# Kernel tuning notes

Measured on AMD Instinct MI355X. Metric: run time of the kernel, lower is better.

Reference implementation:

```python
import jax, jax.numpy as jnp
import numpy as np

NUM_EMBEDDINGS = 1024
EMBEDDING_DIM = 256
COMMITMENT_COST = 0.25


def setup_inputs() -> dict:
    key = jax.random.key(0)
    k1, k2 = jax.random.split(key)
    inputs = jax.random.normal(k1, (32, EMBEDDING_DIM, 32, 32), dtype=jnp.float32)
    # nn.Embedding weight init: uniform(-1/K, 1/K)
    embeddings = (jax.random.uniform(k2, (NUM_EMBEDDINGS, EMBEDDING_DIM), dtype=jnp.float32) * 2.0 - 1.0) / NUM_EMBEDDINGS
    return {"inputs": inputs, "embeddings": embeddings}


def reference(inputs, embeddings):
    B, D, H, W = inputs.shape
    K = embeddings.shape[0]
    # [B,D,H,W] -> [N,D] with N = B*H*W
    flat = jnp.transpose(inputs, (0, 2, 3, 1)).reshape(-1, D)
    distances = (jnp.sum(flat * flat, axis=1, keepdims=True)
                 + jnp.sum(embeddings * embeddings, axis=1)
                 - 2.0 * jnp.matmul(flat, embeddings.T))
    encoding_indices = jnp.argmin(distances, axis=1)  # [N]
    # gather codebook vectors (same math as one-hot @ embeddings)
    quantized = embeddings[encoding_indices]  # [N,D]
    quantized = quantized.reshape(B, H, W, D).transpose(0, 3, 1, 2)  # [B,D,H,W]
    e_latent_loss = jnp.mean((jax.lax.stop_gradient(quantized) - inputs) ** 2)
    q_latent_loss = jnp.mean((quantized - jax.lax.stop_gradient(inputs)) ** 2)
    loss = q_latent_loss + COMMITMENT_COST * e_latent_loss
    # straight-through estimator
    quantized_st = inputs + jax.lax.stop_gradient(quantized - inputs)
    # perplexity from one-hot average (counts / N)
    counts = jnp.zeros((K,), dtype=flat.dtype).at[encoding_indices].add(1.0)
    avg_probs = counts / flat.shape[0]
    perplexity = jnp.exp(-jnp.sum(avg_probs * jnp.log(avg_probs + 1e-10)))
    return quantized_st, loss, perplexity, encoding_indices.reshape(B, H, W)
```

## Files before the change

### kernel.cpp

```cpp
#include <hip/hip_runtime.h>


#define NROWS 32768
#define CAPA 16384
#define CAPB 8192
#define GAP_TAU 1e-4f

typedef __attribute__((ext_vector_type(8))) short short8;
typedef __attribute__((ext_vector_type(8))) unsigned short ushort8;
typedef __attribute__((ext_vector_type(4))) float f32x4;

struct Top4 { float v0, v1, v2, v3; int i0, i1, i2; };

__device__ __forceinline__ void top4_init(Top4& t) {
    t.v0 = t.v1 = t.v2 = t.v3 = 3.4e38f;
    t.i0 = t.i1 = t.i2 = 0x7fffffff;
}
__device__ __forceinline__ void top4_insert(Top4& t, float cv, int ci) {
    if (cv < t.v3) {
        if (cv < t.v2) {
            t.v3 = t.v2;
            if (cv < t.v1) {
                t.v2 = t.v1; t.i2 = t.i1;
                if (cv < t.v0) { t.v1 = t.v0; t.i1 = t.i0; t.v0 = cv; t.i0 = ci; }
                else           { t.v1 = cv; t.i1 = ci; }
            } else { t.v2 = cv; t.i2 = ci; }
        } else { t.v3 = cv; }
    }
}
__device__ __forceinline__ void top4_merge(Top4& t, const Top4& o) {
    top4_insert(t, o.v0, o.i0);
    top4_insert(t, o.v1, o.i1);
    top4_insert(t, o.v2, o.i2);
    t.v3 = fminf(t.v3, o.v3);
}

__device__ __forceinline__ unsigned short bf16_rne(float v) {
    unsigned int u = __float_as_uint(v);
    return (unsigned short)((u + 0x7fffu + ((u >> 16) & 1u)) >> 16);
}
__device__ __forceinline__ float bf16_to_f(unsigned short h) {
    return __uint_as_float(((unsigned int)h) << 16);
}

__device__ __forceinline__ void gl16(const void* g, void* l) {
    __builtin_amdgcn_global_load_lds(
        (const __attribute__((address_space(1))) unsigned int*)g,
        (__attribute__((address_space(3))) unsigned int*)l, 16, 0, 0);
}

template <int STRIDE>
__device__ __forceinline__ float np_sumsq256(const float* __restrict__ p) {
    float half[2];
#pragma unroll
    for (int h = 0; h < 2; ++h) {
        float r[8];
#pragma unroll
        for (int j = 0; j < 8; ++j) {
            const float v = p[(size_t)(h * 128 + j) * STRIDE];
            r[j] = __fmul_rn(v, v);
        }
        for (int i = 8; i < 128; i += 8) {
#pragma unroll
            for (int j = 0; j < 8; ++j) {
                const float v = p[(size_t)(h * 128 + i + j) * STRIDE];
                r[j] = __fadd_rn(r[j], __fmul_rn(v, v));
            }
        }
        half[h] = __fadd_rn(__fadd_rn(__fadd_rn(r[0], r[1]), __fadd_rn(r[2], r[3])),
                            __fadd_rn(__fadd_rn(r[4], r[5]), __fadd_rn(r[6], r[7])));
    }
    return __fadd_rn(half[0], half[1]);
}

__global__ void prep_kernel(const float* __restrict__ emb, const float* __restrict__ x,
                            float* __restrict__ ee, float* __restrict__ xx,
                            unsigned short* __restrict__ EhT, unsigned short* __restrict__ ElT,
                            unsigned short* __restrict__ XhT, unsigned short* __restrict__ XlT,
                            float* __restrict__ wzero) {
    if (blockIdx.x >= 388) {
        for (int i = threadIdx.x; i < 1088; i += 256) wzero[i] = 0.f;
        return;
    }
    if (blockIdx.x < 4) {
        const int k = blockIdx.x * 256 + threadIdx.x;
        ee[k] = np_sumsq256<1>(emb + (size_t)k * 256);
        return;
    }
    if (blockIdx.x >= 260) {
        const int n = (blockIdx.x - 260) * 256 + threadIdx.x;
        const int b = n >> 10, p = n & 1023;
        const float* xb = x + (size_t)b * 262144 + p;
        const int kk = (n >> 1) & 3;
        float r[8];
        float half0 = 0.f, half1 = 0.f;
        for (int dc = 0; dc < 8; ++dc) {
            float v[32];
#pragma unroll
            for (int j = 0; j < 32; ++j)
                v[j] = xb[(size_t)(dc * 32 + j) * 1024];
            if ((dc & 3) == 0) {
#pragma unroll
                for (int j = 0; j < 8; ++j) r[j] = __fmul_rn(v[j], v[j]);
#pragma unroll
                for (int g = 1; g < 4; ++g)
#pragma unroll
                    for (int j = 0; j < 8; ++j)
                        r[j] = __fadd_rn(r[j], __fmul_rn(v[g * 8 + j], v[g * 8 + j]));
            } else {
#pragma unroll
                for (int g = 0; g < 4; ++g)
#pragma unroll
                    for (int j = 0; j < 8; ++j)
                        r[j] = __fadd_rn(r[j], __fmul_rn(v[g * 8 + j], v[g * 8 + j]));
            }
            if ((dc & 3) == 3) {
                const float s = __fadd_rn(
                    __fadd_rn(__fadd_rn(r[0], r[1]), __fadd_rn(r[2], r[3])),
                    __fadd_rn(__fadd_rn(r[4], r[5]), __fadd_rn(r[6], r[7])));
                if (dc == 3) half0 = s; else half1 = s;
            }
            const size_t xrow = ((size_t)dc * NROWS + n) * 32;
#pragma unroll
            for (int g = 0; g < 4; ++g) {
                ushort8 H, L;
#pragma unroll
                for (int j = 0; j < 8; ++j) {
                    const float vv = v[g * 8 + j];
                    const unsigned int u = __float_as_uint(vv);
                    H[j] = (unsigned short)(u >> 16);
                    const float rr = vv - __uint_as_float(u & 0xFFFF0000u);
                    L[j] = (unsigned short)(__float_as_uint(rr) >> 16);
                }
                *(ushort8*)(XhT + xrow + (g ^ kk) * 8) = H;
                *(ushort8*)(XlT + xrow + (g ^ kk) * 8) = L;
            }
        }
        xx[n] = __fadd_rn(half0, half1);
        return;
    }
    const int eid = (blockIdx.x - 4) * 256 + threadIdx.x;
    const int code = eid >> 6;
    const int d0 = (eid & 63) * 4;
    float4 v = *(const float4*)(emb + (size_t)code * 256 + d0);
    const float vv[4] = {v.x, v.y, v.z, v.w};
    unsigned short h[4], l[4];
#pragma unroll
    for (int i = 0; i < 4; ++i) {
        h[i] = bf16_rne(vv[i]);
        l[i] = bf16_rne(vv[i] - bf16_to_f(h[i]));
    }
    const int kk = (code >> 1) & 3;
    const int slot = (d0 & 31) >> 3;
    const int within = (d0 & 31) & 7;
    const size_t o = ((size_t)(d0 >> 5) * 1024 + code) * 32
                   + (size_t)((slot ^ kk) * 8 + within);
    *(ushort4*)(EhT + o) = make_ushort4(h[0], h[1], h[2], h[3]);
    *(ushort4*)(ElT + o) = make_ushort4(l[0], l[1], l[2], l[3]);
}

__global__ __launch_bounds__(256, 2)
void mfma_argmin_kernel(const unsigned short* __restrict__ XhT, const unsigned short* __restrict__ XlT,
                        const unsigned short* __restrict__ EhT, const unsigned short* __restrict__ ElT,
                        const float* __restrict__ ee, const float* __restrict__ xx,
                        float* __restrict__ pv0, float* __restrict__ pv1,
                        float* __restrict__ pv2, float* __restrict__ pv3,
                        int* __restrict__ pi0, int* __restrict__ pi1, int* __restrict__ pi2) {
    __shared__ __attribute__((aligned(16))) unsigned short Eh_s[2][4096];
    __shared__ __attribute__((aligned(16))) unsigned short El_s[2][4096];
    __shared__ __attribute__((aligned(16))) unsigned short Xh_s[2][4096];
    __shared__ __attribute__((aligned(16))) unsigned short Xl_s[2][4096];
    __shared__ float eeLds[128];
    __shared__ float mV0[128], mV1[128], mV2[128], mV3[128];
    __shared__ int   mI0[128], mI1[128], mI2[128];

    const int t = threadIdx.x;
    const int w = t >> 6, lane = t & 63;
    const int lane15 = lane & 15, quad = lane >> 4;
    const int nblk = blockIdx.x & 255, cblk = blockIdx.x >> 8;
    const int n0 = nblk * 128, c0 = cblk * 128;

    if (t < 128) eeLds[t] = ee[c0 + t];

    const int fslot = (quad ^ ((lane15 >> 1) & 3)) * 8;
    int eoffs[4], xoffs[4];
#pragma unroll
    for (int i = 0; i < 4; ++i)
        eoffs[i] = ((w >> 1) * 64 + i * 16 + lane15) * 32 + fslot;
#pragma unroll
    for (int j = 0; j < 4; ++j)
        xoffs[j] = ((w & 1) * 64 + j * 16 + lane15) * 32 + fslot;

    f32x4 acc[4][4];
#pragma unroll
    for (int i = 0; i < 4; ++i)
#pragma unroll
        for (int j = 0; j < 4; ++j) acc[i][j] = (f32x4){0.f, 0.f, 0.f, 0.f};

    auto STAGE = [&](int dc, int bb) {
        const size_t xoff = ((size_t)dc * NROWS + n0) * 32;
        const size_t eoff = ((size_t)dc * 1024 + c0) * 32;
#pragma unroll
        for (int k = 0; k < 2; ++k) {
            const int id = k * 256 + t;
            const int ldso = (k * 256 + w * 64) * 8;
            gl16(XhT + xoff + (size_t)id * 8, &Xh_s[bb][ldso]);
            gl16(XlT + xoff + (size_t)id * 8, &Xl_s[bb][ldso]);
            gl16(EhT + eoff + (size_t)id * 8, &Eh_s[bb][ldso]);
            gl16(ElT + eoff + (size_t)id * 8, &El_s[bb][ldso]);
        }
    };

    STAGE(0, 0);
    asm volatile("s_waitcnt vmcnt(0)" ::: "memory");
    __builtin_amdgcn_s_barrier();
    asm volatile("" ::: "memory");

#pragma unroll 2
    for (int dc = 0; dc < 8; ++dc) {
        const int bb = dc & 1;
        if (dc < 7) STAGE(dc + 1, bb ^ 1);
        short8 ah[4], al[4], bh[4], bl[4];
#pragma unroll
        for (int i = 0; i < 4; ++i) {
            ah[i] = *(const short8*)&Eh_s[bb][eoffs[i]];
            al[i] = *(const short8*)&El_s[bb][eoffs[i]];
        }
#pragma unroll
        for (int j = 0; j < 4; ++j) {
            bh[j] = *(const short8*)&Xh_s[bb][xoffs[j]];
            bl[j] = *(const short8*)&Xl_s[bb][xoffs[j]];
        }
#pragma unroll
        for (int i = 0; i < 4; ++i)
#pragma unroll
            for (int j = 0; j < 4; ++j) {
                acc[i][j] = __builtin_amdgcn_mfma_f32_16x16x32_bf16(al[i], bh[j], acc[i][j], 0, 0, 0);
                acc[i][j] = __builtin_amdgcn_mfma_f32_16x16x32_bf16(ah[i], bl[j], acc[i][j], 0, 0, 0);
                acc[i][j] = __builtin_amdgcn_mfma_f32_16x16x32_bf16(ah[i], bh[j], acc[i][j], 0, 0, 0);
            }
        asm volatile("s_waitcnt vmcnt(0)" ::: "memory");
        __builtin_amdgcn_s_barrier();
        asm volatile("" ::: "memory");
    }

    Top4 tj[4];
#pragma unroll
    for (int j = 0; j < 4; ++j) {
        const float xxv = xx[n0 + (w & 1) * 64 + j * 16 + lane15];
        Top4 tt; top4_init(tt);
#pragma unroll
        for (int i = 0; i < 4; ++i)
#pragma unroll
            for (int r = 0; r < 4; ++r) {
                const int cl = (w >> 1) * 64 + i * 16 + quad * 4 + r;
                const float t1 = __fadd_rn(xxv, eeLds[cl]);
                const float s = __fmaf_rn(-2.0f, acc[i][j][r], t1);
                top4_insert(tt, s, c0 + cl);
            }
#pragma unroll
        for (int off = 16; off <= 32; off <<= 1) {
            Top4 o;
            o.v0 = __shfl_xor(tt.v0, off, 64); o.i0 = __shfl_xor(tt.i0, off, 64);
            o.v1 = __shfl_xor(tt.v1, off, 64); o.i1 = __shfl_xor(tt.i1, off, 64);
            o.v2 = __shfl_xor(tt.v2, off, 64); o.i2 = __shfl_xor(tt.i2, off, 64);
            o.v3 = __shfl_xor(tt.v3, off, 64);
            top4_merge(tt, o);
        }
        tj[j] = tt;
    }
    if (w >= 2 && quad == 0) {
#pragma unroll
        for (int j = 0; j < 4; ++j) {
            const int idx = (w & 1) * 64 + j * 16 + lane15;
            mV0[idx] = tj[j].v0; mV1[idx] = tj[j].v1; mV2[idx] = tj[j].v2; mV3[idx] = tj[j].v3;
            mI0[idx] = tj[j].i0; mI1[idx] = tj[j].i1; mI2[idx] = tj[j].i2;
        }
    }
    __syncthreads();
    if (w < 2 && quad == 0) {
#pragma unroll
        for (int j = 0; j < 4; ++j) {
            const int idx = w * 64 + j * 16 + lane15;
            Top4 tt = tj[j];
            Top4 o;
            o.v0 = mV0[idx]; o.v1 = mV1[idx]; o.v2 = mV2[idx]; o.v3 = mV3[idx];
            o.i0 = mI0[idx]; o.i1 = mI1[idx]; o.i2 = mI2[idx];
            top4_merge(tt, o);
            mV0[idx] = tt.v0; mV1[idx] = tt.v1; mV2[idx] = tt.v2; mV3[idx] = tt.v3;
            mI0[idx] = tt.i0; mI1[idx] = tt.i1; mI2[idx] = tt.i2;
        }
    }
    __syncthreads();
    if (t < 128) {
        const size_t g = (size_t)cblk * NROWS + n0 + t;
        pv0[g] = mV0[t]; pv1[g] = mV1[t]; pv2[g] = mV2[t]; pv3[g] = mV3[t];
        pi0[g] = mI0[t]; pi1[g] = mI1[t]; pi2[g] = mI2[t];
    }
}

__global__ void combine_kernel(const float* __restrict__ pv0, const float* __restrict__ pv1,
                               const float* __restrict__ pv2, const float* __restrict__ pv3,
                               const int* __restrict__ pi0, const int* __restrict__ pi1,
                               const int* __restrict__ pi2,
                               int* __restrict__ fidx, float* __restrict__ outIdx,
                               int* __restrict__ counts,
                               int* __restrict__ listA, int* __restrict__ nA,
                               int* __restrict__ listB, int* __restrict__ nB) {
    const int n = blockIdx.x * blockDim.x + threadIdx.x;
    if (n >= NROWS) return;
    float v0[8], v1[8], v2[8]; int i0[8], i1[8], i2[8];
    float b1 = 3.4e38f, v4m = 3.4e38f;
#pragma unroll
    for (int s = 0; s < 8; ++s) {
        const size_t g = (size_t)s * NROWS + n;
        v0[s] = pv0[g]; v1[s] = pv1[g]; v2[s] = pv2[g];
        i0[s] = pi0[g]; i1[s] = pi1[g]; i2[s] = pi2[g];
        b1 = fminf(b1, v0[s]);
        v4m = fminf(v4m, pv3[g]);
    }
    if (v4m - b1 < GAP_TAU) {
        const int s = atomicAdd(nB, 1);
        if (s < CAPB) { listB[s] = n; return; }
    } else {
        int ks[24]; int cnt = 0;
#pragma unroll
        for (int s = 0; s < 8; ++s) {
            if (v0[s] - b1 < GAP_TAU) ks[cnt++] = i0[s];
            if (v1[s] - b1 < GAP_TAU) ks[cnt++] = i1[s];
            if (v2[s] - b1 < GAP_TAU) ks[cnt++] = i2[s];
        }
        if (cnt > 1) {
            const int slot = atomicAdd(nA, 1);
            if (slot < CAPA) {
                int* e = listA + (size_t)slot * 32;
                e[0] = n; e[1] = cnt;
                for (int c = 0; c < cnt; ++c) e[2 + c] = ks[c];
                return;
            }
            const int s2 = atomicAdd(nB, 1);
            if (s2 < CAPB) { listB[s2] = n; return; }
        }
        const int bi = ks[0];
        fidx[n] = bi;
        outIdx[n] = (float)bi;
        atomicAdd(&counts[bi], 1);
        return;
    }
    int bi = 0x7fffffff;
#pragma unroll
    for (int s = 0; s < 8; ++s) if (v0[s] == b1 && i0[s] < bi) bi = i0[s];
    fidx[n] = bi; outIdx[n] = (float)bi; atomicAdd(&counts[bi], 1);
}

__global__ __launch_bounds__(256)
void resolve_kernel(const float* __restrict__ x, const float* __restrict__ emb,
                    const float* __restrict__ ee, const float* __restrict__ xx,
                    const int* __restrict__ listA, const int* __restrict__ nA,
                    const int* __restrict__ listB, const int* __restrict__ nB,
                    int* __restrict__ fidx, float* __restrict__ outIdx,
                    int* __restrict__ counts) {
    __shared__ float xrow[256];
    __shared__ float bV[4];
    __shared__ int   bI[4];
    if (blockIdx.x < 512) {
        int total = *nA; if (total > CAPA) total = CAPA;
        const int sub = threadIdx.x >> 5;
        const int li  = threadIdx.x & 31;
        for (int e = blockIdx.x * 8 + sub; e < total; e += 512 * 8) {
            const int* ent = listA + (size_t)e * 32;
            const int n = ent[0], cnt = ent[1];
            float s = 3.4e38f; int k = 0x7fffffff;
            if (li < cnt) {
                k = ent[2 + li];
                const int b = n >> 10, p = n & 1023;
                const float* xr = x + (size_t)b * 262144 + p;
                const float* er = emb + (size_t)k * 256;
                float dot = 0.f;
#pragma unroll 8
                for (int d = 0; d < 256; ++d)
                    dot = __fmaf_rn(er[d], xr[(size_t)d * 1024], dot);
                s = __fmaf_rn(-2.0f, dot, __fadd_rn(xx[n], ee[k]));
            }
#pragma unroll
            for (int off = 1; off < 32; off <<= 1) {
                const float ov = __shfl_xor(s, off, 32);
                const int   ok = __shfl_xor(k, off, 32);
                if (ov < s || (ov == s && ok < k)) { s = ov; k = ok; }
            }
            if (li == 0) { fidx[n] = k; outIdx[n] = (float)k; atomicAdd(&counts[k], 1); }
        }
        return;
    }
    int total = *nB; if (total > CAPB) total = CAPB;
    for (int wq = (int)blockIdx.x - 512; wq < total; wq += 64) {
        const int n = listB[wq];
        const int b = n >> 10, p = n & 1023;
        const float* xb = x + (size_t)b * 262144 + p;
        xrow[threadIdx.x] = xb[(size_t)threadIdx.x * 1024];
        __syncthreads();
        const float xxn = xx[n];
        float best = 3.4e38f; int bi = 0x7fffffff;
        for (int k = threadIdx.x; k < 1024; k += 256) {
            const float* e = emb + (size_t)k * 256;
            float dot = 0.f;
            for (int d = 0; d < 256; ++d) dot = __fmaf_rn(e[d], xrow[d], dot);
            const float t1 = __fadd_rn(xxn, ee[k]);
            const float s = __fmaf_rn(-2.0f, dot, t1);
            if (s < best) { best = s; bi = k; }
        }
        for (int off = 32; off > 0; off >>= 1) {
            const float ov = __shfl_down(best, off, 64);
            const int   oi = __shfl_down(bi,   off, 64);
            if (ov < best || (ov == best && oi < bi)) { best = ov; bi = oi; }
        }
        const int lane = threadIdx.x & 63, wv = threadIdx.x >> 6;
        if (lane == 0) { bV[wv] = best; bI[wv] = bi; }
        __syncthreads();
        if (threadIdx.x == 0) {
            float bb = bV[0]; int ii = bI[0];
            for (int i = 1; i < 4; ++i)
                if (bV[i] < bb || (bV[i] == bb && bI[i] < ii)) { bb = bV[i]; ii = bI[i]; }
            fidx[n] = ii;
            outIdx[n] = (float)ii;
            atomicAdd(&counts[ii], 1);
        }
        __syncthreads();
    }
}

__global__ __launch_bounds__(256)
void quantize_kernel(const float* __restrict__ x, const float* __restrict__ emb,
                     const int* __restrict__ fidx, float* __restrict__ out,
                     float* __restrict__ sumsq) {
    const int tid = blockIdx.x * 256 + threadIdx.x;
    const int dchunk = tid >> 15;
    const int n = tid & 32767;
    const int b = n >> 10, p = n & 1023;
    const int d0 = dchunk * 64;
    const int k = fidx[n];
    const float4* er = (const float4*)(emb + (size_t)k * 256 + d0);
    const float* xr = x + (size_t)b * 262144 + (size_t)d0 * 1024 + p;
    float* orow = out + (size_t)b * 262144 + (size_t)d0 * 1024 + p;
    float loc = 0.f;
#pragma unroll
    for (int j = 0; j < 16; ++j) {
        const float4 qv = er[j];
        const float q[4] = {qv.x, qv.y, qv.z, qv.w};
#pragma unroll
        for (int i = 0; i < 4; ++i) {
            const size_t off = (size_t)(j * 4 + i) * 1024;
            const float xv = xr[off];
            const float e = q[i] - xv;
            orow[off] = xv + e;
            loc = fmaf(e, e, loc);
        }
    }
    for (int off = 32; off > 0; off >>= 1) loc += __shfl_down(loc, off, 64);
    __shared__ float red[4];
    const int lane = threadIdx.x & 63, wv = threadIdx.x >> 6;
    if (lane == 0) red[wv] = loc;
    __syncthreads();
    if (threadIdx.x == 0) atomicAdd(sumsq, red[0] + red[1] + red[2] + red[3]);
}

__global__ void finalize_kernel(const int* __restrict__ counts, const float* __restrict__ sumsq,
                                float* __restrict__ outScalars) {
    const int k = threadIdx.x;
    const float p = (float)counts[k] * (1.0f / 32768.0f);
    float term = p * logf(p + 1e-10f);
    for (int off = 32; off > 0; off >>= 1) term += __shfl_down(term, off, 64);
    __shared__ float red[16];
    const int lane = k & 63, wv = k >> 6;
    if (lane == 0) red[wv] = term;
    __syncthreads();
    if (k == 0) {
        float s = 0.f;
        for (int i = 0; i < 16; ++i) s += red[i];
        const float m = sumsq[0] * (1.0f / 8388608.0f);
        outScalars[0] = 1.25f * m;
        outScalars[1] = expf(-s);
    }
}

extern "C" void kernel_launch(void* const* d_in, const int* in_sizes, int n_in,
                              void* d_out, int out_size, void* d_ws, size_t ws_size,
                              hipStream_t stream) {
    const float* x   = (const float*)d_in[0];
    const float* emb = (const float*)d_in[1];
    float* out = (float*)d_out;
    float* W   = (float*)d_ws;
    float* sumsq = W;
    int*   nA    = (int*)(W + 1);
    int*   nB    = (int*)(W + 2);
    int*   counts = (int*)(W + 64);
    float* ee    = W + 1088;
    float* xx    = W + 2112;
    float* pv0   = W + 34880;
    float* pv1   = W + 297024;
    float* pv2   = W + 559168;
    float* pv3   = W + 821312;
    int*   pi0   = (int*)(W + 1083456);
    int*   pi1   = (int*)(W + 1345600);
    int*   pi2   = (int*)(W + 1607744);
    int*   listA = (int*)(W + 1869888);
    int*   listB = (int*)(W + 2394176);
    unsigned short* EhT = (unsigned short*)(W + 2402368);
    unsigned short* ElT = (unsigned short*)(W + 2533440);
    int*   fidx  = (int*)(W + 2664512);
    unsigned short* XhT = (unsigned short*)(W + 2697280);
    unsigned short* XlT = (unsigned short*)(W + 6891584);

    prep_kernel<<<389, 256, 0, stream>>>(emb, x, ee, xx, EhT, ElT, XhT, XlT, W);
    mfma_argmin_kernel<<<2048, 256, 0, stream>>>(XhT, XlT, EhT, ElT, ee, xx,
                                                 pv0, pv1, pv2, pv3, pi0, pi1, pi2);
    combine_kernel<<<128, 256, 0, stream>>>(pv0, pv1, pv2, pv3, pi0, pi1, pi2,
                                            fidx, out + 8388610, counts, listA, nA, listB, nB);
    resolve_kernel<<<576, 256, 0, stream>>>(x, emb, ee, xx, listA, nA, listB, nB,
                                            fidx, out + 8388610, counts);
    quantize_kernel<<<512, 256, 0, stream>>>(x, emb, fidx, out, sumsq);
    finalize_kernel<<<1, 1024, 0, stream>>>(counts, sumsq, out + 8388608);
}
```

Before: 234.2 us.

## Drop LDS double buffering and raise occupancy target to four blocks

Replaces the double-buffered LDS staging of the X and E bf16 hi/lo tiles with a single buffer and plain barriers before and after each load. This halves shared memory per block, and the launch bound is raised from 2 to 4 blocks per CU so more blocks can hide latency instead of software prefetching. It also adds a barrier before the cross-wave top-4 merge. The cost is that global loads no longer overlap MFMA work within a block, and the tighter register budget risks spilling the 64-register accumulator tile.

```diff
diff --git a/kernel.cpp b/kernel.cpp
--- a/kernel.cpp
+++ b/kernel.cpp
@@ -159,17 +159,17 @@
     *(ushort4*)(ElT + o) = make_ushort4(l[0], l[1], l[2], l[3]);
 }
 
-__global__ __launch_bounds__(256, 2)
+__global__ __launch_bounds__(256, 4)
 void mfma_argmin_kernel(const unsigned short* __restrict__ XhT, const unsigned short* __restrict__ XlT,
                         const unsigned short* __restrict__ EhT, const unsigned short* __restrict__ ElT,
                         const float* __restrict__ ee, const float* __restrict__ xx,
                         float* __restrict__ pv0, float* __restrict__ pv1,
                         float* __restrict__ pv2, float* __restrict__ pv3,
                         int* __restrict__ pi0, int* __restrict__ pi1, int* __restrict__ pi2) {
-    __shared__ __attribute__((aligned(16))) unsigned short Eh_s[2][4096];
-    __shared__ __attribute__((aligned(16))) unsigned short El_s[2][4096];
-    __shared__ __attribute__((aligned(16))) unsigned short Xh_s[2][4096];
-    __shared__ __attribute__((aligned(16))) unsigned short Xl_s[2][4096];
+    __shared__ __attribute__((aligned(16))) unsigned short Eh_s[4096];
+    __shared__ __attribute__((aligned(16))) unsigned short El_s[4096];
+    __shared__ __attribute__((aligned(16))) unsigned short Xh_s[4096];
+    __shared__ __attribute__((aligned(16))) unsigned short Xl_s[4096];
     __shared__ float eeLds[128];
     __shared__ float mV0[128], mV1[128], mV2[128], mV3[128];
     __shared__ int   mI0[128], mI1[128], mI2[128];
@@ -197,39 +197,30 @@
 #pragma unroll
         for (int j = 0; j < 4; ++j) acc[i][j] = (f32x4){0.f, 0.f, 0.f, 0.f};
 
-    auto STAGE = [&](int dc, int bb) {
+    for (int dc = 0; dc < 8; ++dc) {
+        if (dc) __syncthreads();
         const size_t xoff = ((size_t)dc * NROWS + n0) * 32;
         const size_t eoff = ((size_t)dc * 1024 + c0) * 32;
 #pragma unroll
         for (int k = 0; k < 2; ++k) {
             const int id = k * 256 + t;
             const int ldso = (k * 256 + w * 64) * 8;
-            gl16(XhT + xoff + (size_t)id * 8, &Xh_s[bb][ldso]);
-            gl16(XlT + xoff + (size_t)id * 8, &Xl_s[bb][ldso]);
-            gl16(EhT + eoff + (size_t)id * 8, &Eh_s[bb][ldso]);
-            gl16(ElT + eoff + (size_t)id * 8, &El_s[bb][ldso]);
-        }
-    };
-
-    STAGE(0, 0);
-    asm volatile("s_waitcnt vmcnt(0)" ::: "memory");
-    __builtin_amdgcn_s_barrier();
-    asm volatile("" ::: "memory");
-
-#pragma unroll 2
-    for (int dc = 0; dc < 8; ++dc) {
-        const int bb = dc & 1;
-        if (dc < 7) STAGE(dc + 1, bb ^ 1);
+            gl16(XhT + xoff + (size_t)id * 8, &Xh_s[ldso]);
+            gl16(XlT + xoff + (size_t)id * 8, &Xl_s[ldso]);
+            gl16(EhT + eoff + (size_t)id * 8, &Eh_s[ldso]);
+            gl16(ElT + eoff + (size_t)id * 8, &El_s[ldso]);
+        }
+        __syncthreads();
         short8 ah[4], al[4], bh[4], bl[4];
 #pragma unroll
         for (int i = 0; i < 4; ++i) {
-            ah[i] = *(const short8*)&Eh_s[bb][eoffs[i]];
-            al[i] = *(const short8*)&El_s[bb][eoffs[i]];
+            ah[i] = *(const short8*)&Eh_s[eoffs[i]];
+            al[i] = *(const short8*)&El_s[eoffs[i]];
         }
 #pragma unroll
         for (int j = 0; j < 4; ++j) {
-            bh[j] = *(const short8*)&Xh_s[bb][xoffs[j]];
-            bl[j] = *(const short8*)&Xl_s[bb][xoffs[j]];
+            bh[j] = *(const short8*)&Xh_s[xoffs[j]];
+            bl[j] = *(const short8*)&Xl_s[xoffs[j]];
         }
 #pragma unroll
         for (int i = 0; i < 4; ++i)
@@ -239,9 +230,6 @@
                 acc[i][j] = __builtin_amdgcn_mfma_f32_16x16x32_bf16(ah[i], bl[j], acc[i][j], 0, 0, 0);
                 acc[i][j] = __builtin_amdgcn_mfma_f32_16x16x32_bf16(ah[i], bh[j], acc[i][j], 0, 0, 0);
             }
-        asm volatile("s_waitcnt vmcnt(0)" ::: "memory");
-        __builtin_amdgcn_s_barrier();
-        asm volatile("" ::: "memory");
     }
 
     Top4 tj[4];
@@ -269,6 +257,7 @@
         }
         tj[j] = tt;
     }
+    __syncthreads();
     if (w >= 2 && quad == 0) {
 #pragma unroll
         for (int j = 0; j < 4; ++j) {
```

Result: faster. 214.5 us (-8.4%).
